# Performance work log

Hardware: AMD Instinct MI355X
Metric: run time of the kernel (lower is better)

## Reference

```python
import jax, jax.numpy as jnp
import numpy as np

B, S, F = 512, 512, 128   # batch, seq_len, facts_size (= querry_size)
H1, H2 = 80, 40
PAD = float(-2**32 + 1)


def setup_inputs() -> dict:
    key = jax.random.key(0)
    ks = jax.random.split(key, 12)
    inp = {
        "query": jax.random.normal(ks[0], (B, F), jnp.float32),
        "facts": jax.random.normal(ks[1], (B, S, F), jnp.float32),
        "mask": jax.random.randint(ks[2], (B, S), 0, 2, jnp.int32),
        # mlp1: querry_size -> facts_size
        "W1": jax.random.normal(ks[3], (F, F), jnp.float32) / np.sqrt(F),
        "b1": jnp.zeros((F,), jnp.float32),
        # PReLU alpha (per-feature, init zeros)
        "alpha": jnp.zeros((F,), jnp.float32),
        # mlp2: 4*F -> 80
        "W2": jax.random.normal(ks[4], (4 * F, H1), jnp.float32) / np.sqrt(4 * F),
        "b2": jnp.zeros((H1,), jnp.float32),
        # mlp3: 80 -> 40
        "W3": jax.random.normal(ks[5], (H1, H2), jnp.float32) / np.sqrt(H1),
        "b3": jnp.zeros((H2,), jnp.float32),
        # mlp4: 40 -> 1
        "W4": jax.random.normal(ks[6], (H2, 1), jnp.float32) / np.sqrt(H2),
        "b4": jnp.zeros((1,), jnp.float32),
    }
    return inp


def reference(query, facts, mask, W1, b1, alpha, W2, b2, W3, b3, W4, b4):
    # mlp1 + PReLU on the query
    q = query @ W1 + b1                                   # [B, F]
    q = jnp.where(q >= 0, q, alpha * q)                   # PReLU, alpha per-feature
    # broadcast query over sequence (tile+reshape in the original)
    qs = jnp.broadcast_to(q[:, None, :], (q.shape[0], S, F))  # [B, S, F]
    din = jnp.concatenate([qs, facts, qs - facts, qs * facts], axis=-1)  # [B,S,4F]
    h1 = jax.nn.sigmoid(din @ W2 + b2)                    # [B, S, 80]
    h2 = jax.nn.sigmoid(h1 @ W3 + b3)                     # [B, S, 40]
    scores = (h2 @ W4 + b4)[..., 0][:, None, :]           # [B, 1, S]
    key_masks = (mask == 1)[:, None, :]                   # [B, 1, S]
    scores = jnp.where(key_masks, scores, PAD)
    scores = jax.nn.softmax(scores, axis=-1)              # softmax over seq
    out = jnp.einsum("bqs,bsf->bqf", scores, facts)       # [B, 1, F]  (mode SUM)
    return out
```

## Files before the change

### kernel.cpp

```cpp
#include <hip/hip_runtime.h>
#include <hip/hip_bf16.h>

typedef __bf16 bf16x8 __attribute__((ext_vector_type(8)));
typedef float  f32x4  __attribute__((ext_vector_type(4)));

#define WBT_STRIDE 136
#define H1_STRIDE  104
#define W3T_STRIDE 104

__global__ __launch_bounds__(256, 2)
void attn_fcn_kernel(const float* __restrict__ query,
                     const float* __restrict__ facts,
                     const int*   __restrict__ mask,
                     const float* __restrict__ W1,
                     const float* __restrict__ b1,
                     const float* __restrict__ alpha,
                     const float* __restrict__ W2,
                     const float* __restrict__ b2,
                     const float* __restrict__ W3,
                     const float* __restrict__ b3,
                     const float* __restrict__ W4,
                     const float* __restrict__ b4,
                     float* __restrict__ out)
{
    __shared__ float  qy[128];
    __shared__ float  qs[128];
    __shared__ float  qconst[80];
    __shared__ __align__(16) __bf16 WbT[80 * WBT_STRIDE];
    __shared__ __align__(16) __bf16 W3T[48 * W3T_STRIDE];
    __shared__ __align__(16) __bf16 h1sB[4][16 * H1_STRIDE];
    __shared__ float  sc16[4][16];
    __shared__ float  outacc[4][128];
    __shared__ float  MZ[4][2];
    __shared__ float  w4s[48];
    __shared__ float  b3s[48];

    const int b = blockIdx.x;
    const int t = threadIdx.x;

    if (t < 128) qy[t] = query[b * 128 + t];
    for (int e = t; e < 48 * W3T_STRIDE; e += 256) W3T[e] = (__bf16)0.0f;
    for (int e = t; e < 4 * 16 * H1_STRIDE; e += 256) (&h1sB[0][0])[e] = (__bf16)0.0f;
    if (t < 48) {
        w4s[t] = (t < 40) ? W4[t] : 0.0f;
        b3s[t] = (t < 40) ? b3[t] : 0.0f;
    }
    __syncthreads();

    for (int e = t; e < 80 * 40; e += 256) {
        int k = e / 40, j = e % 40;
        W3T[j * W3T_STRIDE + k] = (__bf16)W3[e];
    }
    if (t < 128) {
        float acc = b1[t];
        #pragma unroll 4
        for (int k = 0; k < 128; ++k) acc = fmaf(qy[k], W1[k * 128 + t], acc);
        float a = alpha[t];
        qs[t] = (acc >= 0.0f) ? acc : a * acc;
    }
    __syncthreads();

    if (t < 80) {
        float acc = b2[t];
        #pragma unroll 4
        for (int k = 0; k < 128; ++k)
            acc = fmaf(qs[k], W2[k * 80 + t] + W2[(256 + k) * 80 + t], acc);
        qconst[t] = acc;
    }
    for (int e = t; e < 128 * 80; e += 256) {
        int k = e / 80, n = e % 80;
        float w = W2[(128 + k) * 80 + n] - W2[(256 + k) * 80 + n]
                + qs[k] * W2[(384 + k) * 80 + n];
        WbT[n * WBT_STRIDE + k] = (__bf16)w;
    }
    __syncthreads();

    const int wave = t >> 6;
    const int lane = t & 63;
    const int qd   = lane >> 4;
    const int m    = lane & 15;
    const float b4v = b4[0];
    const float* fb = facts + (size_t)b * (512 * 128);
    const int*   mb = mask + b * 512;
    __bf16* h1w = &h1sB[wave][0];

    bf16x8 w3f[3][3];
    #pragma unroll
    for (int ct = 0; ct < 3; ++ct)
        #pragma unroll
        for (int kc = 0; kc < 3; ++kc)
            w3f[ct][kc] = *(const bf16x8*)&W3T[(ct * 16 + m) * W3T_STRIDE + kc * 32 + qd * 8];

    float Mrun = -INFINITY, Zrun = 0.0f;
    float oacc[4][8];
    #pragma unroll
    for (int kc = 0; kc < 4; ++kc)
        #pragma unroll
        for (int i = 0; i < 8; ++i) oacc[kc][i] = 0.0f;

    for (int tile = 0; tile < 8; ++tile) {
        const int s0 = wave * 128 + tile * 16;

        f32x4 av[4][2];
        #pragma unroll
        for (int kc = 0; kc < 4; ++kc) {
            const float* p = &fb[(size_t)(s0 + m) * 128 + kc * 32 + qd * 8];
            av[kc][0] = *(const f32x4*)p;
            av[kc][1] = *(const f32x4*)(p + 4);
        }
        bf16x8 af[4];
        #pragma unroll
        for (int kc = 0; kc < 4; ++kc)
            #pragma unroll
            for (int i = 0; i < 8; ++i)
                af[kc][i] = (__bf16)((i < 4) ? av[kc][0][i] : av[kc][1][i - 4]);

        #pragma unroll
        for (int ct = 0; ct < 5; ++ct) {
            f32x4 acc = {0.f, 0.f, 0.f, 0.f};
            #pragma unroll
            for (int kc = 0; kc < 4; ++kc) {
                bf16x8 bfr = *(const bf16x8*)&WbT[(ct * 16 + m) * WBT_STRIDE + kc * 32 + qd * 8];
                acc = __builtin_amdgcn_mfma_f32_16x16x32_bf16(af[kc], bfr, acc, 0, 0, 0);
            }
            const int col = ct * 16 + m;
            const float qc = qconst[col];
            #pragma unroll
            for (int r = 0; r < 4; ++r) {
                float x = acc[r] + qc;
                float h = __builtin_amdgcn_rcpf(1.0f + __expf(-x));
                h1w[(qd * 4 + r) * H1_STRIDE + col] = (__bf16)h;
            }
        }
        asm volatile("s_waitcnt lgkmcnt(0)" ::: "memory");

        bf16x8 a2[3];
        #pragma unroll
        for (int kc = 0; kc < 3; ++kc)
            a2[kc] = *(const bf16x8*)&h1w[m * H1_STRIDE + kc * 32 + qd * 8];
        float sc[4] = {0.f, 0.f, 0.f, 0.f};
        #pragma unroll
        for (int ct = 0; ct < 3; ++ct) {
            f32x4 acc2 = {0.f, 0.f, 0.f, 0.f};
            #pragma unroll
            for (int kc = 0; kc < 3; ++kc)
                acc2 = __builtin_amdgcn_mfma_f32_16x16x32_bf16(a2[kc], w3f[ct][kc], acc2, 0, 0, 0);
            const int col = ct * 16 + m;
            const float w4v = w4s[col], b3v = b3s[col];
            #pragma unroll
            for (int r = 0; r < 4; ++r) {
                float h2 = __builtin_amdgcn_rcpf(1.0f + __expf(-(acc2[r] + b3v)));
                sc[r] = fmaf(h2, w4v, sc[r]);
            }
        }
        #pragma unroll
        for (int d = 1; d < 16; d <<= 1)
            #pragma unroll
            for (int r = 0; r < 4; ++r)
                sc[r] += __shfl_xor(sc[r], d);
        if (m == 0) {
            #pragma unroll
            for (int r = 0; r < 4; ++r) {
                const int row = qd * 4 + r;
                float v = sc[r] + b4v;
                if (mb[s0 + row] != 1) v = -INFINITY;
                sc16[wave][row] = v;
            }
        }
        asm volatile("s_waitcnt lgkmcnt(0)" ::: "memory");

        float tmax = -INFINITY;
        #pragma unroll
        for (int i = 0; i < 16; ++i) tmax = fmaxf(tmax, sc16[wave][i]);
        float Mn = fmaxf(Mrun, tmax);
        float alph, pm, tsum;
        if (Mn == -INFINITY) {
            alph = 1.0f; pm = 0.0f; tsum = 0.0f;
        } else {
            alph = __expf(Mrun - Mn);
            tsum = 0.0f;
            #pragma unroll
            for (int i = 0; i < 16; ++i) tsum += __expf(sc16[wave][i] - Mn);
            pm = __expf(sc16[wave][m] - Mn);
        }
        Zrun = Zrun * alph + tsum;
        Mrun = Mn;
        #pragma unroll
        for (int kc = 0; kc < 4; ++kc) {
            #pragma unroll
            for (int i = 0; i < 4; ++i) {
                oacc[kc][i]     = fmaf(pm, av[kc][0][i], oacc[kc][i]     * alph);
                oacc[kc][i + 4] = fmaf(pm, av[kc][1][i], oacc[kc][i + 4] * alph);
            }
        }
    }

    #pragma unroll
    for (int d = 1; d < 16; d <<= 1)
        #pragma unroll
        for (int kc = 0; kc < 4; ++kc)
            #pragma unroll
            for (int i = 0; i < 8; ++i)
                oacc[kc][i] += __shfl_xor(oacc[kc][i], d);
    if (m == 0) {
        #pragma unroll
        for (int kc = 0; kc < 4; ++kc)
            #pragma unroll
            for (int i = 0; i < 8; ++i)
                outacc[wave][kc * 32 + qd * 8 + i] = oacc[kc][i];
        if (lane == 0) { MZ[wave][0] = Mrun; MZ[wave][1] = Zrun; }
    }
    __syncthreads();

    if (t < 128) {
        float Mg = fmaxf(fmaxf(MZ[0][0], MZ[1][0]), fmaxf(MZ[2][0], MZ[3][0]));
        float Zg = 0.0f, val = 0.0f;
        #pragma unroll
        for (int w = 0; w < 4; ++w) {
            float swt = __expf(MZ[w][0] - Mg);
            Zg  = fmaf(MZ[w][1], swt, Zg);
            val = fmaf(outacc[w][t], swt, val);
        }
        out[b * 128 + t] = val / Zg;
    }
}

extern "C" void kernel_launch(void* const* d_in, const int* in_sizes, int n_in,
                              void* d_out, int out_size, void* d_ws, size_t ws_size,
                              hipStream_t stream) {
    (void)in_sizes; (void)n_in; (void)d_ws; (void)ws_size; (void)out_size;
    const float* query = (const float*)d_in[0];
    const float* facts = (const float*)d_in[1];
    const int*   mask  = (const int*)d_in[2];
    const float* W1 = (const float*)d_in[3];
    const float* b1 = (const float*)d_in[4];
    const float* al = (const float*)d_in[5];
    const float* W2 = (const float*)d_in[6];
    const float* b2 = (const float*)d_in[7];
    const float* W3 = (const float*)d_in[8];
    const float* b3 = (const float*)d_in[9];
    const float* W4 = (const float*)d_in[10];
    const float* b4 = (const float*)d_in[11];
    attn_fcn_kernel<<<dim3(512), dim3(256), 0, stream>>>(
        query, facts, mask, W1, b1, al, W2, b2, W3, b3, W4, b4, (float*)d_out);
}
```

Measured before the change: 257.9 us.

## Use 512-thread blocks, prefetch facts tiles, and replace online softmax with two-pass

Doubles the block to 8 waves so each wave scores 64 rows instead of 128. The next facts tile is prefetched into registers while the current one is computed. The per-tile online softmax is replaced by a block-wide max/sum reduction over all 512 scores, followed by a second pass that re-reads facts from global memory for the weighted sum. This cuts per-wave serial latency and register pressure (W3 fragments are now loaded from LDS instead of held in registers), at the cost of reading facts a second time and adding extra block barriers.

```diff
diff --git a/kernel.cpp b/kernel.cpp
--- a/kernel.cpp
+++ b/kernel.cpp
@@ -8,7 +8,7 @@
 #define H1_STRIDE  104
 #define W3T_STRIDE 104
 
-__global__ __launch_bounds__(256, 2)
+__global__ __launch_bounds__(512, 4)
 void attn_fcn_kernel(const float* __restrict__ query,
                      const float* __restrict__ facts,
                      const int*   __restrict__ mask,
@@ -26,28 +26,29 @@
     __shared__ float  qy[128];
     __shared__ float  qs[128];
     __shared__ float  qconst[80];
+    __shared__ float  w4s[48];
+    __shared__ float  b3s[48];
     __shared__ __align__(16) __bf16 WbT[80 * WBT_STRIDE];
     __shared__ __align__(16) __bf16 W3T[48 * W3T_STRIDE];
-    __shared__ __align__(16) __bf16 h1sB[4][16 * H1_STRIDE];
-    __shared__ float  sc16[4][16];
+    __shared__ __align__(16) __bf16 h1sB[8][16 * H1_STRIDE];
+    __shared__ float  scores[512];
+    __shared__ float  wred[8];
+    __shared__ float  wsum[8];
     __shared__ float  outacc[4][128];
-    __shared__ float  MZ[4][2];
-    __shared__ float  w4s[48];
-    __shared__ float  b3s[48];
 
     const int b = blockIdx.x;
     const int t = threadIdx.x;
 
     if (t < 128) qy[t] = query[b * 128 + t];
-    for (int e = t; e < 48 * W3T_STRIDE; e += 256) W3T[e] = (__bf16)0.0f;
-    for (int e = t; e < 4 * 16 * H1_STRIDE; e += 256) (&h1sB[0][0])[e] = (__bf16)0.0f;
+    for (int e = t; e < 48 * W3T_STRIDE; e += 512) W3T[e] = (__bf16)0.0f;
+    for (int e = t; e < 8 * 16 * H1_STRIDE; e += 512) (&h1sB[0][0])[e] = (__bf16)0.0f;
     if (t < 48) {
         w4s[t] = (t < 40) ? W4[t] : 0.0f;
         b3s[t] = (t < 40) ? b3[t] : 0.0f;
     }
     __syncthreads();
 
-    for (int e = t; e < 80 * 40; e += 256) {
+    for (int e = t; e < 80 * 40; e += 512) {
         int k = e / 40, j = e % 40;
         W3T[j * W3T_STRIDE + k] = (__bf16)W3[e];
     }
@@ -67,7 +68,7 @@
             acc = fmaf(qs[k], W2[k * 80 + t] + W2[(256 + k) * 80 + t], acc);
         qconst[t] = acc;
     }
-    for (int e = t; e < 128 * 80; e += 256) {
+    for (int e = t; e < 128 * 80; e += 512) {
         int k = e / 80, n = e % 80;
         float w = W2[(128 + k) * 80 + n] - W2[(256 + k) * 80 + n]
                 + qs[k] * W2[(384 + k) * 80 + n];
@@ -79,41 +80,39 @@
     const int lane = t & 63;
     const int qd   = lane >> 4;
     const int m    = lane & 15;
-    const float b4v = b4[0];
     const float* fb = facts + (size_t)b * (512 * 128);
     const int*   mb = mask + b * 512;
     __bf16* h1w = &h1sB[wave][0];
-
-    bf16x8 w3f[3][3];
-    #pragma unroll
-    for (int ct = 0; ct < 3; ++ct)
-        #pragma unroll
-        for (int kc = 0; kc < 3; ++kc)
-            w3f[ct][kc] = *(const bf16x8*)&W3T[(ct * 16 + m) * W3T_STRIDE + kc * 32 + qd * 8];
-
-    float Mrun = -INFINITY, Zrun = 0.0f;
-    float oacc[4][8];
-    #pragma unroll
-    for (int kc = 0; kc < 4; ++kc)
-        #pragma unroll
-        for (int i = 0; i < 8; ++i) oacc[kc][i] = 0.0f;
-
-    for (int tile = 0; tile < 8; ++tile) {
-        const int s0 = wave * 128 + tile * 16;
-
-        f32x4 av[4][2];
+    const int wbase = wave * 64;
+
+    f32x4 av[4][2];
+    {
+        const float* p0 = &fb[(size_t)(wbase + m) * 128 + qd * 8];
         #pragma unroll
         for (int kc = 0; kc < 4; ++kc) {
-            const float* p = &fb[(size_t)(s0 + m) * 128 + kc * 32 + qd * 8];
-            av[kc][0] = *(const f32x4*)p;
-            av[kc][1] = *(const f32x4*)(p + 4);
-        }
+            av[kc][0] = *(const f32x4*)(p0 + kc * 32);
+            av[kc][1] = *(const f32x4*)(p0 + kc * 32 + 4);
+        }
+    }
+
+    for (int tile = 0; tile < 4; ++tile) {
+        const int s0 = wbase + tile * 16;
+
         bf16x8 af[4];
         #pragma unroll
         for (int kc = 0; kc < 4; ++kc)
             #pragma unroll
             for (int i = 0; i < 8; ++i)
                 af[kc][i] = (__bf16)((i < 4) ? av[kc][0][i] : av[kc][1][i - 4]);
+
+        if (tile < 3) {
+            const float* pn = &fb[(size_t)(s0 + 16 + m) * 128 + qd * 8];
+            #pragma unroll
+            for (int kc = 0; kc < 4; ++kc) {
+                av[kc][0] = *(const f32x4*)(pn + kc * 32);
+                av[kc][1] = *(const f32x4*)(pn + kc * 32 + 4);
+            }
+        }
 
         #pragma unroll
         for (int ct = 0; ct < 5; ++ct) {
@@ -143,8 +142,10 @@
         for (int ct = 0; ct < 3; ++ct) {
             f32x4 acc2 = {0.f, 0.f, 0.f, 0.f};
             #pragma unroll
-            for (int kc = 0; kc < 3; ++kc)
-                acc2 = __builtin_amdgcn_mfma_f32_16x16x32_bf16(a2[kc], w3f[ct][kc], acc2, 0, 0, 0);
+            for (int kc = 0; kc < 3; ++kc) {
+                bf16x8 bfr = *(const bf16x8*)&W3T[(ct * 16 + m) * W3T_STRIDE + kc * 32 + qd * 8];
+                acc2 = __builtin_amdgcn_mfma_f32_16x16x32_bf16(a2[kc], bfr, acc2, 0, 0, 0);
+            }
             const int col = ct * 16 + m;
             const float w4v = w4s[col], b3v = b3s[col];
             #pragma unroll
@@ -160,69 +161,53 @@
                 sc[r] += __shfl_xor(sc[r], d);
         if (m == 0) {
             #pragma unroll
-            for (int r = 0; r < 4; ++r) {
-                const int row = qd * 4 + r;
-                float v = sc[r] + b4v;
-                if (mb[s0 + row] != 1) v = -INFINITY;
-                sc16[wave][row] = v;
-            }
-        }
-        asm volatile("s_waitcnt lgkmcnt(0)" ::: "memory");
-
-        float tmax = -INFINITY;
-        #pragma unroll
-        for (int i = 0; i < 16; ++i) tmax = fmaxf(tmax, sc16[wave][i]);
-        float Mn = fmaxf(Mrun, tmax);
-        float alph, pm, tsum;
-        if (Mn == -INFINITY) {
-            alph = 1.0f; pm = 0.0f; tsum = 0.0f;
-        } else {
-            alph = __expf(Mrun - Mn);
-            tsum = 0.0f;
-            #pragma unroll
-            for (int i = 0; i < 16; ++i) tsum += __expf(sc16[wave][i] - Mn);
-            pm = __expf(sc16[wave][m] - Mn);
-        }
-        Zrun = Zrun * alph + tsum;
-        Mrun = Mn;
-        #pragma unroll
-        for (int kc = 0; kc < 4; ++kc) {
-            #pragma unroll
-            for (int i = 0; i < 4; ++i) {
-                oacc[kc][i]     = fmaf(pm, av[kc][0][i], oacc[kc][i]     * alph);
-                oacc[kc][i + 4] = fmaf(pm, av[kc][1][i], oacc[kc][i + 4] * alph);
-            }
-        }
-    }
-
-    #pragma unroll
-    for (int d = 1; d < 16; d <<= 1)
-        #pragma unroll
-        for (int kc = 0; kc < 4; ++kc)
-            #pragma unroll
-            for (int i = 0; i < 8; ++i)
-                oacc[kc][i] += __shfl_xor(oacc[kc][i], d);
-    if (m == 0) {
-        #pragma unroll
-        for (int kc = 0; kc < 4; ++kc)
-            #pragma unroll
-            for (int i = 0; i < 8; ++i)
-                outacc[wave][kc * 32 + qd * 8 + i] = oacc[kc][i];
-        if (lane == 0) { MZ[wave][0] = Mrun; MZ[wave][1] = Zrun; }
-    }
-    __syncthreads();
-
-    if (t < 128) {
-        float Mg = fmaxf(fmaxf(MZ[0][0], MZ[1][0]), fmaxf(MZ[2][0], MZ[3][0]));
-        float Zg = 0.0f, val = 0.0f;
-        #pragma unroll
-        for (int w = 0; w < 4; ++w) {
-            float swt = __expf(MZ[w][0] - Mg);
-            Zg  = fmaf(MZ[w][1], swt, Zg);
-            val = fmaf(outacc[w][t], swt, val);
-        }
-        out[b * 128 + t] = val / Zg;
-    }
+            for (int r = 0; r < 4; ++r)
+                scores[s0 + qd * 4 + r] = sc[r];
+        }
+    }
+    __syncthreads();
+
+    const float b4v = b4[0];
+    float v = scores[t] + b4v;
+    if (mb[t] != 1) v = -INFINITY;
+    float r = v;
+    #pragma unroll
+    for (int d = 1; d < 64; d <<= 1) r = fmaxf(r, __shfl_xor(r, d));
+    if (lane == 0) wred[wave] = r;
+    __syncthreads();
+    float gmax = wred[0];
+    #pragma unroll
+    for (int w = 1; w < 8; ++w) gmax = fmaxf(gmax, wred[w]);
+    float e = (gmax == -INFINITY) ? 1.0f : __expf(v - gmax);
+    float z = e;
+    #pragma unroll
+    for (int d = 1; d < 64; d <<= 1) z += __shfl_xor(z, d);
+    if (lane == 0) wsum[wave] = z;
+    scores[t] = e;
+    __syncthreads();
+    float Zg = wsum[0];
+    #pragma unroll
+    for (int w = 1; w < 8; ++w) Zg += wsum[w];
+
+    {
+        const int f   = t & 127;
+        const int qtr = t >> 7;
+        const float* fp = fb + (size_t)qtr * 128 * 128 + f;
+        const float* pp = &scores[qtr * 128];
+        float a0 = 0.f, a1 = 0.f, a2 = 0.f, a3 = 0.f;
+        #pragma unroll 4
+        for (int s = 0; s < 128; s += 4) {
+            a0 = fmaf(pp[s],     fp[(size_t)(s)     * 128], a0);
+            a1 = fmaf(pp[s + 1], fp[(size_t)(s + 1) * 128], a1);
+            a2 = fmaf(pp[s + 2], fp[(size_t)(s + 2) * 128], a2);
+            a3 = fmaf(pp[s + 3], fp[(size_t)(s + 3) * 128], a3);
+        }
+        outacc[qtr][f] = (a0 + a1) + (a2 + a3);
+    }
+    __syncthreads();
+    if (t < 128)
+        out[b * 128 + t] =
+            ((outacc[0][t] + outacc[1][t]) + (outacc[2][t] + outacc[3][t])) / Zg;
 }
 
 extern "C" void kernel_launch(void* const* d_in, const int* in_sizes, int n_in,
@@ -241,6 +226,6 @@
     const float* b3 = (const float*)d_in[9];
     const float* W4 = (const float*)d_in[10];
     const float* b4 = (const float*)d_in[11];
-    attn_fcn_kernel<<<dim3(512), dim3(256), 0, stream>>>(
+    attn_fcn_kernel<<<dim3(512), dim3(512), 0, stream>>>(
         query, facts, mask, W1, b1, al, W2, b2, W3, b3, W4, b4, (float*)d_out);
 }
```

New measurement: 256.7 us. About the same (-0.5%).

## Split into prep, split-sequence main, and combine kernels with max-free softmax

Applied to the files above, without the earlier changes.

Moves the per-batch query MLP and folded W2 weight preparation into a separate prep kernel that writes bf16 weights to workspace. The main kernel splits each batch's sequence across two blocks (1024 blocks, higher occupancy bound), streams W3 from global, and drops the running-max softmax in favour of plain exp sums, also dropping b4 since it cancels. A small combine kernel merges the two halves and normalizes. This trades extra launches and workspace traffic for more parallelism and less per-block serial prep; removing max subtraction risks overflow if scores grow large.

```diff
diff --git a/kernel.cpp b/kernel.cpp
--- a/kernel.cpp
+++ b/kernel.cpp
@@ -6,72 +6,119 @@
 
 #define WBT_STRIDE 136
 #define H1_STRIDE  104
-#define W3T_STRIDE 104
-
-__global__ __launch_bounds__(256, 2)
-void attn_fcn_kernel(const float* __restrict__ query,
-                     const float* __restrict__ facts,
-                     const int*   __restrict__ mask,
-                     const float* __restrict__ W1,
-                     const float* __restrict__ b1,
-                     const float* __restrict__ alpha,
-                     const float* __restrict__ W2,
-                     const float* __restrict__ b2,
-                     const float* __restrict__ W3,
-                     const float* __restrict__ b3,
-                     const float* __restrict__ W4,
-                     const float* __restrict__ b4,
-                     float* __restrict__ out)
+
+#define WS_WBT   0u
+#define WS_QC    10485760u
+#define WS_W3T   10649600u
+#define WS_OP    10658816u
+#define WS_Z     11183104u
+
+__global__ __launch_bounds__(256)
+void k1_prep(const float* __restrict__ query,
+             const float* __restrict__ W1, const float* __restrict__ b1,
+             const float* __restrict__ alpha,
+             const float* __restrict__ W2, const float* __restrict__ b2,
+             const float* __restrict__ W3,
+             unsigned char* __restrict__ ws)
 {
-    __shared__ float  qy[128];
-    __shared__ float  qs[128];
-    __shared__ float  qconst[80];
-    __shared__ __align__(16) __bf16 WbT[80 * WBT_STRIDE];
-    __shared__ __align__(16) __bf16 W3T[48 * W3T_STRIDE];
-    __shared__ __align__(16) __bf16 h1sB[4][16 * H1_STRIDE];
-    __shared__ float  sc16[4][16];
-    __shared__ float  outacc[4][128];
-    __shared__ float  MZ[4][2];
-    __shared__ float  w4s[48];
-    __shared__ float  b3s[48];
+    __shared__ float qy[128];
+    __shared__ float qpart[2][128];
+    __shared__ float qs[128];
+    __shared__ float qcp[2][80];
 
     const int b = blockIdx.x;
     const int t = threadIdx.x;
+    __hip_bfloat16* wbt = (__hip_bfloat16*)(ws + WS_WBT);
+    float*          qcw = (float*)(ws + WS_QC);
+    __hip_bfloat16* w3t = (__hip_bfloat16*)(ws + WS_W3T);
 
     if (t < 128) qy[t] = query[b * 128 + t];
-    for (int e = t; e < 48 * W3T_STRIDE; e += 256) W3T[e] = (__bf16)0.0f;
-    for (int e = t; e < 4 * 16 * H1_STRIDE; e += 256) (&h1sB[0][0])[e] = (__bf16)0.0f;
+    __syncthreads();
+
+    {
+        const int j = t & 127, kh = t >> 7;
+        float acc = (kh == 0) ? b1[j] : 0.0f;
+        const float* w1p = W1 + (kh * 64) * 128 + j;
+        #pragma unroll 4
+        for (int k = 0; k < 64; ++k) acc = fmaf(qy[kh * 64 + k], w1p[k * 128], acc);
+        qpart[kh][j] = acc;
+    }
+    if (b == 0) {
+        for (int e = t; e < 48 * 96; e += 256) {
+            int j = e / 96, k = e % 96;
+            float v = (j < 40 && k < 80) ? W3[k * 40 + j] : 0.0f;
+            w3t[e] = __hip_bfloat16(v);
+        }
+    }
+    __syncthreads();
+    if (t < 128) {
+        float s = qpart[0][t] + qpart[1][t];
+        float a = alpha[t];
+        qs[t] = (s >= 0.0f) ? s : a * s;
+    }
+    __syncthreads();
+
+    if (t < 160) {
+        const int jj = (t < 80) ? t : t - 80;
+        const int hh = (t < 80) ? 0 : 1;
+        float acc = (hh == 0) ? b2[jj] : 0.0f;
+        #pragma unroll 4
+        for (int k = hh * 64; k < hh * 64 + 64; ++k)
+            acc = fmaf(qs[k], W2[k * 80 + jj] + W2[(256 + k) * 80 + jj], acc);
+        qcp[hh][jj] = acc;
+    }
+    for (int e = t; e < 128 * 80; e += 256) {
+        int k = e / 80, n = e - k * 80;
+        float w = W2[(128 + k) * 80 + n] - W2[(256 + k) * 80 + n]
+                + qs[k] * W2[(384 + k) * 80 + n];
+        wbt[b * 10240 + e] = __hip_bfloat16(w);
+    }
+    __syncthreads();
+    if (t < 80) qcw[b * 80 + t] = qcp[0][t] + qcp[1][t];
+}
+
+__global__ __launch_bounds__(256, 4)
+void k2_main(const float* __restrict__ facts,
+             const int*   __restrict__ mask,
+             const float* __restrict__ W4, const float* __restrict__ b3,
+             unsigned char* __restrict__ ws)
+{
+    __shared__ __align__(16) __bf16 WbT[80 * WBT_STRIDE];
+    __shared__ __align__(16) __bf16 h1sB[4][16 * H1_STRIDE];
+    __shared__ float qcs[80];
+    __shared__ float w4s[48];
+    __shared__ float b3s[48];
+    __shared__ float sc16[4][16];
+    __shared__ float outacc[4][128];
+    __shared__ float Zw[4];
+
+    const int b2 = blockIdx.x;
+    const int batch = b2 >> 1;
+    const int half  = b2 & 1;
+    const int t = threadIdx.x;
+
+    const __hip_bfloat16* wbt = (const __hip_bfloat16*)(ws + WS_WBT) + batch * 10240;
+    const float*          qcw = (const float*)(ws + WS_QC) + batch * 80;
+    const __bf16*         w3t = (const __bf16*)(ws + WS_W3T);
+    float*                opw = (float*)(ws + WS_OP);
+    float*                zpw = (float*)(ws + WS_Z);
+
+    #pragma unroll
+    for (int i = 0; i < 5; ++i) {
+        int elem = (t + i * 256) * 8;
+        bf16x8 v = *(const bf16x8*)&wbt[elem];
+        int k = elem / 80, n = elem - k * 80;
+        #pragma unroll
+        for (int j = 0; j < 8; ++j) WbT[(n + j) * WBT_STRIDE + k] = v[j];
+    }
+    for (int e = t; e < 64 * 16; e += 256) {
+        int r = e >> 4, c = 80 + (e & 15);
+        (&h1sB[0][0])[r * H1_STRIDE + c] = (__bf16)0.0f;
+    }
+    if (t < 80) qcs[t] = qcw[t];
     if (t < 48) {
         w4s[t] = (t < 40) ? W4[t] : 0.0f;
         b3s[t] = (t < 40) ? b3[t] : 0.0f;
-    }
-    __syncthreads();
-
-    for (int e = t; e < 80 * 40; e += 256) {
-        int k = e / 40, j = e % 40;
-        W3T[j * W3T_STRIDE + k] = (__bf16)W3[e];
-    }
-    if (t < 128) {
-        float acc = b1[t];
-        #pragma unroll 4
-        for (int k = 0; k < 128; ++k) acc = fmaf(qy[k], W1[k * 128 + t], acc);
-        float a = alpha[t];
-        qs[t] = (acc >= 0.0f) ? acc : a * acc;
-    }
-    __syncthreads();
-
-    if (t < 80) {
-        float acc = b2[t];
-        #pragma unroll 4
-        for (int k = 0; k < 128; ++k)
-            acc = fmaf(qs[k], W2[k * 80 + t] + W2[(256 + k) * 80 + t], acc);
-        qconst[t] = acc;
-    }
-    for (int e = t; e < 128 * 80; e += 256) {
-        int k = e / 80, n = e % 80;
-        float w = W2[(128 + k) * 80 + n] - W2[(256 + k) * 80 + n]
-                + qs[k] * W2[(384 + k) * 80 + n];
-        WbT[n * WBT_STRIDE + k] = (__bf16)w;
     }
     __syncthreads();
 
@@ -79,34 +126,30 @@
     const int lane = t & 63;
     const int qd   = lane >> 4;
     const int m    = lane & 15;
-    const float b4v = b4[0];
-    const float* fb = facts + (size_t)b * (512 * 128);
-    const int*   mb = mask + b * 512;
+    const float* fb = facts + (size_t)batch * (512 * 128);
+    const int*   mb = mask + batch * 512;
     __bf16* h1w = &h1sB[wave][0];
-
-    bf16x8 w3f[3][3];
-    #pragma unroll
-    for (int ct = 0; ct < 3; ++ct)
-        #pragma unroll
-        for (int kc = 0; kc < 3; ++kc)
-            w3f[ct][kc] = *(const bf16x8*)&W3T[(ct * 16 + m) * W3T_STRIDE + kc * 32 + qd * 8];
-
-    float Mrun = -INFINITY, Zrun = 0.0f;
+    const int sbase = half * 256 + wave * 64;
+
     float oacc[4][8];
     #pragma unroll
     for (int kc = 0; kc < 4; ++kc)
         #pragma unroll
         for (int i = 0; i < 8; ++i) oacc[kc][i] = 0.0f;
-
-    for (int tile = 0; tile < 8; ++tile) {
-        const int s0 = wave * 128 + tile * 16;
+    float Zl = 0.0f;
+
+    for (int tile = 0; tile < 4; ++tile) {
+        const int s0 = sbase + tile * 16;
+        const int mv = mb[s0 + m];
 
         f32x4 av[4][2];
-        #pragma unroll
-        for (int kc = 0; kc < 4; ++kc) {
-            const float* p = &fb[(size_t)(s0 + m) * 128 + kc * 32 + qd * 8];
-            av[kc][0] = *(const f32x4*)p;
-            av[kc][1] = *(const f32x4*)(p + 4);
+        {
+            const float* p0 = &fb[(size_t)(s0 + m) * 128 + qd * 8];
+            #pragma unroll
+            for (int kc = 0; kc < 4; ++kc) {
+                av[kc][0] = *(const f32x4*)(p0 + kc * 32);
+                av[kc][1] = *(const f32x4*)(p0 + kc * 32 + 4);
+            }
         }
         bf16x8 af[4];
         #pragma unroll
@@ -124,7 +167,7 @@
                 acc = __builtin_amdgcn_mfma_f32_16x16x32_bf16(af[kc], bfr, acc, 0, 0, 0);
             }
             const int col = ct * 16 + m;
-            const float qc = qconst[col];
+            const float qc = qcs[col];
             #pragma unroll
             for (int r = 0; r < 4; ++r) {
                 float x = acc[r] + qc;
@@ -143,8 +186,10 @@
         for (int ct = 0; ct < 3; ++ct) {
             f32x4 acc2 = {0.f, 0.f, 0.f, 0.f};
             #pragma unroll
-            for (int kc = 0; kc < 3; ++kc)
-                acc2 = __builtin_amdgcn_mfma_f32_16x16x32_bf16(a2[kc], w3f[ct][kc], acc2, 0, 0, 0);
+            for (int kc = 0; kc < 3; ++kc) {
+                bf16x8 bfr = *(const bf16x8*)&w3t[(ct * 16 + m) * 96 + kc * 32 + qd * 8];
+                acc2 = __builtin_amdgcn_mfma_f32_16x16x32_bf16(a2[kc], bfr, acc2, 0, 0, 0);
+            }
             const int col = ct * 16 + m;
             const float w4v = w4s[col], b3v = b3s[col];
             #pragma unroll
@@ -160,75 +205,63 @@
                 sc[r] += __shfl_xor(sc[r], d);
         if (m == 0) {
             #pragma unroll
-            for (int r = 0; r < 4; ++r) {
-                const int row = qd * 4 + r;
-                float v = sc[r] + b4v;
-                if (mb[s0 + row] != 1) v = -INFINITY;
-                sc16[wave][row] = v;
-            }
+            for (int r = 0; r < 4; ++r) sc16[wave][qd * 4 + r] = sc[r];
         }
         asm volatile("s_waitcnt lgkmcnt(0)" ::: "memory");
 
-        float tmax = -INFINITY;
-        #pragma unroll
-        for (int i = 0; i < 16; ++i) tmax = fmaxf(tmax, sc16[wave][i]);
-        float Mn = fmaxf(Mrun, tmax);
-        float alph, pm, tsum;
-        if (Mn == -INFINITY) {
-            alph = 1.0f; pm = 0.0f; tsum = 0.0f;
-        } else {
-            alph = __expf(Mrun - Mn);
-            tsum = 0.0f;
-            #pragma unroll
-            for (int i = 0; i < 16; ++i) tsum += __expf(sc16[wave][i] - Mn);
-            pm = __expf(sc16[wave][m] - Mn);
-        }
-        Zrun = Zrun * alph + tsum;
-        Mrun = Mn;
-        #pragma unroll
-        for (int kc = 0; kc < 4; ++kc) {
+        const float pm = (mv == 1) ? __expf(sc16[wave][m]) : 0.0f;
+        Zl += pm;
+        #pragma unroll
+        for (int kc = 0; kc < 4; ++kc)
             #pragma unroll
             for (int i = 0; i < 4; ++i) {
-                oacc[kc][i]     = fmaf(pm, av[kc][0][i], oacc[kc][i]     * alph);
-                oacc[kc][i + 4] = fmaf(pm, av[kc][1][i], oacc[kc][i + 4] * alph);
-            }
-        }
+                oacc[kc][i]     = fmaf(pm, av[kc][0][i], oacc[kc][i]);
+                oacc[kc][i + 4] = fmaf(pm, av[kc][1][i], oacc[kc][i + 4]);
+            }
     }
 
     #pragma unroll
-    for (int d = 1; d < 16; d <<= 1)
+    for (int d = 1; d < 16; d <<= 1) {
         #pragma unroll
         for (int kc = 0; kc < 4; ++kc)
             #pragma unroll
             for (int i = 0; i < 8; ++i)
                 oacc[kc][i] += __shfl_xor(oacc[kc][i], d);
+        Zl += __shfl_xor(Zl, d);
+    }
     if (m == 0) {
         #pragma unroll
         for (int kc = 0; kc < 4; ++kc)
             #pragma unroll
             for (int i = 0; i < 8; ++i)
                 outacc[wave][kc * 32 + qd * 8 + i] = oacc[kc][i];
-        if (lane == 0) { MZ[wave][0] = Mrun; MZ[wave][1] = Zrun; }
-    }
-    __syncthreads();
-
-    if (t < 128) {
-        float Mg = fmaxf(fmaxf(MZ[0][0], MZ[1][0]), fmaxf(MZ[2][0], MZ[3][0]));
-        float Zg = 0.0f, val = 0.0f;
-        #pragma unroll
-        for (int w = 0; w < 4; ++w) {
-            float swt = __expf(MZ[w][0] - Mg);
-            Zg  = fmaf(MZ[w][1], swt, Zg);
-            val = fmaf(outacc[w][t], swt, val);
-        }
-        out[b * 128 + t] = val / Zg;
-    }
+        if (lane == 0) Zw[wave] = Zl;
+    }
+    __syncthreads();
+
+    if (t < 128)
+        opw[(size_t)b2 * 128 + t] =
+            ((outacc[0][t] + outacc[1][t]) + (outacc[2][t] + outacc[3][t]));
+    if (t == 0)
+        zpw[b2] = (Zw[0] + Zw[1]) + (Zw[2] + Zw[3]);
+}
+
+__global__ __launch_bounds__(256)
+void k3_combine(const unsigned char* __restrict__ ws, float* __restrict__ out)
+{
+    const float* opw = (const float*)(ws + WS_OP);
+    const float* zpw = (const float*)(ws + WS_Z);
+    int g = blockIdx.x * 256 + threadIdx.x;
+    int b = g >> 7, f = g & 127;
+    float o = opw[(size_t)(2 * b) * 128 + f] + opw[(size_t)(2 * b + 1) * 128 + f];
+    float Z = zpw[2 * b] + zpw[2 * b + 1];
+    out[g] = o / Z;
 }
 
 extern "C" void kernel_launch(void* const* d_in, const int* in_sizes, int n_in,
                               void* d_out, int out_size, void* d_ws, size_t ws_size,
                               hipStream_t stream) {
-    (void)in_sizes; (void)n_in; (void)d_ws; (void)ws_size; (void)out_size;
+    (void)in_sizes; (void)n_in; (void)ws_size; (void)out_size;
     const float* query = (const float*)d_in[0];
     const float* facts = (const float*)d_in[1];
     const int*   mask  = (const int*)d_in[2];
@@ -241,6 +274,10 @@
     const float* b3 = (const float*)d_in[9];
     const float* W4 = (const float*)d_in[10];
     const float* b4 = (const float*)d_in[11];
-    attn_fcn_kernel<<<dim3(512), dim3(256), 0, stream>>>(
-        query, facts, mask, W1, b1, al, W2, b2, W3, b3, W4, b4, (float*)d_out);
-}
+    (void)b4;
+    unsigned char* ws = (unsigned char*)d_ws;
+
+    k1_prep<<<dim3(512), dim3(256), 0, stream>>>(query, W1, b1, al, W2, b2, W3, ws);
+    k2_main<<<dim3(1024), dim3(256), 0, stream>>>(facts, mask, W4, b3, ws);
+    k3_combine<<<dim3(256), dim3(256), 0, stream>>>(ws, (float*)d_out);
+}
```

After: 249.9 us. -3.1%, faster.
